# Optimization experiments

Hardware: AMD Instinct MI355X
Metric: run time of the kernel (lower is better)

Reference implementation:

```python
import jax, jax.numpy as jnp
import numpy as np

B, L, N = 16, 512, 32          # batch, seq_length, feature_size
E = 128                        # embed_size == frequency_size (number_frequency=1)
EMB = 8                        # embedding_dim
FCH = 64                       # fc_hidden_dim
H = 256                        # hidden_size
PRE = 96                       # pre_length
LAMBDA = 0.01                  # sparsity_threshold
SCALE = 0.02                   # init_scale


def softshrink(v, lambd=LAMBDA):
    return jnp.where(v > lambd, v - lambd, jnp.where(v < -lambd, v + lambd, 0.0))


def setup_inputs() -> dict:
    key = jax.random.key(0)
    ks = jax.random.split(key, 16)
    f32 = jnp.float32
    return {
        "x": jax.random.normal(ks[0], (B, L, N), f32),
        "emb": jax.random.normal(ks[1], (1, E), f32),
        "w0": SCALE * jax.random.normal(ks[2], (2, E, E), f32),
        "b0": SCALE * jax.random.normal(ks[3], (2, E), f32),
        "w1": SCALE * jax.random.normal(ks[4], (2, E, E), f32),
        "b1": SCALE * jax.random.normal(ks[5], (2, E), f32),
        "w2": SCALE * jax.random.normal(ks[6], (2, E, E), f32),
        "b2": SCALE * jax.random.normal(ks[7], (2, E), f32),
        "emb10": jax.random.normal(ks[8], (L, EMB), f32),
        "fc1_w": jax.random.normal(ks[9], (FCH, E * EMB), f32) / np.sqrt(E * EMB),
        "fc1_b": jnp.zeros((FCH,), f32),
        "fc2_w": jax.random.normal(ks[10], (H, FCH), f32) / np.sqrt(FCH),
        "fc2_b": jnp.zeros((H,), f32),
        "fc3_w": jax.random.normal(ks[11], (PRE, H), f32) / np.sqrt(H),
        "fc3_b": jnp.zeros((PRE,), f32),
    }


def _diag(w):
    # einsum 'bli,ii->bli' multiplies by the DIAGONAL of w only
    return jnp.diagonal(w, axis1=-2, axis2=-1)


def reference(x, emb, w0, b0, w1, b1, w2, b2, emb10,
              fc1_w, fc1_b, fc2_w, fc2_b, fc3_w, fc3_b):
    Bb = x.shape[0]
    xt = jnp.transpose(x, (0, 2, 1)).reshape(Bb, -1)          # [B, N*L]
    tok = xt[:, :, None] * emb                                 # [B, N*L, E]
    xf = jnp.fft.rfft(tok, axis=1, norm="ortho")               # [B, N*L//2+1, E] complex
    bias = xf

    # --- fourierGC (faithful to the torch op ordering, incl. o_real reuse) ---
    relu = jax.nn.relu
    d00, d01 = _diag(w0[0]), _diag(w0[1])
    o_r = relu(xf.real * d00 - xf.imag * d01 + b0[0])
    o_i = relu(xf.imag * d00 + xf.real * d01 + b0[1])
    prev = softshrink(jnp.stack([o_r, o_i], axis=-1))

    # middle layer (num_layers=3 -> one): note o_i uses the UPDATED o_r, as in torch
    d10, d11 = _diag(w1[0]), _diag(w1[1])
    o_r_new = relu(o_r * d10 - o_i * d11 + b1[0])
    o_i = relu(o_i * d10 + o_r_new * d11 + b1[1])
    o_r = o_r_new
    prev = softshrink(jnp.stack([o_r, o_i], axis=-1)) + prev

    # last layer
    d20, d21 = _diag(w2[0]), _diag(w2[1])
    o_r_new = relu(o_r * d20 - o_i * d21 + b2[0])
    o_i = relu(o_i * d20 + o_r_new * d21 + b2[1])
    z = softshrink(jnp.stack([o_r_new, o_i], axis=-1)) + prev
    zc = jax.lax.complex(z[..., 0], z[..., 1])

    xf = zc + bias
    xt = jnp.fft.irfft(xf, n=N * L, axis=1, norm="ortho")      # [B, N*L, E]
    xt = xt.reshape(Bb, N, L, E)
    xt = jnp.transpose(xt, (0, 1, 3, 2))                        # [B, N, E, L]
    h = jnp.matmul(xt, emb10)                                   # [B, N, E, EMB]
    h = h.reshape(Bb, N, E * EMB)

    lrelu = lambda v: jax.nn.leaky_relu(v, 0.01)
    h = lrelu(h @ fc1_w.T + fc1_b)
    h = lrelu(h @ fc2_w.T + fc2_b)
    out = h @ fc3_w.T + fc3_b                                   # [B, N, PRE]
    return out[:, 0, :]                                         # target_idx = 0
```

## Files before the change

### kernel.cpp

```cpp
#include <hip/hip_runtime.h>
#include <math.h>

#define Bsz   16
#define Lseq  512
#define Nfeat 32
#define E     128
#define EMB   8
#define FCH   64
#define Hd    256
#define PRE   96
#define M     16384
#define MH    8193
#define LAMBDA 0.01f

#define OFF_CS  0
#define OFF_P   131088

#define REV_M   6.103515625e-5f
#define REV_128 7.8125e-3f

__device__ __forceinline__ float sin_rev(float r) { return __builtin_amdgcn_sinf(r); }
__device__ __forceinline__ float cos_rev(float r) { return __builtin_amdgcn_cosf(r); }

__global__ __launch_bounds__(256, 4)
void k_cs(const float* __restrict__ emb10, float* __restrict__ ws) {
  __shared__ float e10T[Lseq * EMB];
  int bid = blockIdx.x, tid = threadIdx.x;
  for (int j = tid; j < Lseq * EMB; j += 256) {
    int t = j >> 3, m = j & 7;
    e10T[m * 512 + t] = emb10[j];
  }
  __syncthreads();
  int floc = tid >> 5, tl = tid & 31;
  #pragma unroll
  for (int ff = 0; ff < 4; ++ff) {
    int f = bid * 32 + ff * 8 + floc;
    float ca[EMB], sa[EMB];
    #pragma unroll
    for (int m = 0; m < EMB; ++m) { ca[m] = 0.f; sa[m] = 0.f; }
    #pragma unroll 4
    for (int it = 0; it < 16; ++it) {
      int t = tl + 32 * it;
      int k = (f * t) & (M - 1);
      float rv = (float)k * REV_M;
      float cc = cos_rev(rv), ss = sin_rev(rv);
      #pragma unroll
      for (int m = 0; m < EMB; ++m) {
        float ev = e10T[m * 512 + t];
        ca[m] = fmaf(cc, ev, ca[m]);
        sa[m] = fmaf(ss, ev, sa[m]);
      }
    }
    #pragma unroll
    for (int off = 16; off >= 1; off >>= 1) {
      #pragma unroll
      for (int m = 0; m < EMB; ++m) {
        ca[m] += __shfl_xor(ca[m], off, 64);
        sa[m] += __shfl_xor(sa[m], off, 64);
      }
    }
    if (tl == 0) {
      float wf = (f == 0) ? (1.0f / 128.0f) : (2.0f / 128.0f);
      float* o = ws + OFF_CS + f * 16;
      #pragma unroll
      for (int m = 0; m < EMB; ++m) { o[m] = ca[m] * wf; o[8 + m] = sa[m] * wf; }
    }
  }
  if (bid == 0 && tid < 64) {
    int m = tid & 7, g = tid >> 3;
    float p = 0.f;
    #pragma unroll 8
    for (int j = 0; j < 64; ++j) p += e10T[m * 512 + g + 8 * j];
    p = (g & 1) ? -p : p;
    p += __shfl_xor(p, 8, 64);
    p += __shfl_xor(p, 16, 64);
    p += __shfl_xor(p, 32, 64);
    if (g == 0) {
      ws[OFF_CS + 8192 * 16 + m] = p * (1.0f / 128.0f);
      ws[OFF_CS + 8192 * 16 + 8 + m] = 0.f;
    }
  }
}

#define XPAD(t) ((t) + ((t) >> 9))
__global__ __launch_bounds__(1024, 8)
void k_gcf(const float* __restrict__ x, const float* __restrict__ emb,
           const float* __restrict__ w0, const float* __restrict__ b0,
           const float* __restrict__ w1, const float* __restrict__ b1,
           const float* __restrict__ w2, const float* __restrict__ b2,
           float* __restrict__ ws) {
  __shared__ __align__(16) float xf[16416];
  __shared__ __align__(16) float2 Gs[4 * 132];
  float2* Xs = (float2*)xf;
  float* red = xf + 1024;
  int f1g = blockIdx.x, b = blockIdx.y, tid = threadIdx.x;
  int f1base = f1g * 4;
  {
    const float* xb = x + b * (Lseq * Nfeat);
    #pragma unroll
    for (int i = tid; i < Lseq * Nfeat; i += 1024) {
      int l = i >> 5, n = i & 31;
      xf[n * 513 + l] = xb[i];
    }
  }
  __syncthreads();
  if (tid < 512) {
    int f1loc = tid >> 7, t1 = tid & 127;
    int f1 = f1base + f1loc;
    float s1 = sin_rev((float)f1 * REV_128), c1 = cos_rev((float)f1 * REV_128);
    float c2 = c1 * c1 - s1 * s1, s2 = 2.f * s1 * c1;
    float cA = 1.f, sA = 0.f, cB = c1, sB = s1;
    float grA = 0.f, giA = 0.f, grB = 0.f, giB = 0.f;
    #pragma unroll 8
    for (int t2 = 0; t2 < 128; t2 += 2) {
      int ta = t1 + 128 * t2;
      float x0 = xf[XPAD(ta)], x1 = xf[XPAD(ta + 128)];
      grA = fmaf(x0, cA, grA); giA = fmaf(x0, -sA, giA);
      grB = fmaf(x1, cB, grB); giB = fmaf(x1, -sB, giB);
      float cn = cA * c2 - sA * s2; sA = sA * c2 + cA * s2; cA = cn;
      cn = cB * c2 - sB * s2;       sB = sB * c2 + cB * s2; cB = cn;
    }
    float gr = grA + grB, gi = giA + giB;
    float rv = (float)(f1 * t1) * REV_M;
    float sb = sin_rev(rv), cb = cos_rev(rv);
    Gs[f1loc * 132 + (t1 >> 5) * 33 + (t1 & 31)] =
        make_float2(gr * cb + gi * sb, gi * cb - gr * sb);
  }
  __syncthreads();
  {
    int w = tid >> 6, lane = tid & 63;
    int f1loc = w >> 2;
    int q = lane >> 4, f2 = ((w & 3) << 4) + (lane & 15);
    int r = (f2 * q) & 3;
    float c = (r == 0) ? 1.f : (r == 2) ? -1.f : 0.f;
    float s = (r == 1) ? 1.f : (r == 3) ? -1.f : 0.f;
    float s1 = sin_rev((float)f2 * REV_128), c1 = cos_rev((float)f2 * REV_128);
    float xr = 0.f, xi = 0.f;
    const float2* g = Gs + f1loc * 132 + q * 33;
    #pragma unroll 8
    for (int k = 0; k < 32; ++k) {
      float2 gv = g[k];
      xr = fmaf(gv.x, c, xr); xr = fmaf(gv.y, s, xr);
      xi = fmaf(gv.y, c, xi); xi = fmaf(-gv.x, s, xi);
      float cn = c * c1 - s * s1; s = s * c1 + c * s1; c = cn;
    }
    xr += __shfl_xor(xr, 16, 64); xi += __shfl_xor(xi, 16, 64);
    xr += __shfl_xor(xr, 32, 64); xi += __shfl_xor(xi, 32, 64);
    if (lane < 16) Xs[f1loc * 64 + f2] = make_float2(xr, xi);
    if (f1base == 0 && tid < 64) {
      int t1v = tid * 2;
      const float2* g0p = Gs + (t1v >> 5) * 33;
      float2 g0 = g0p[t1v & 31], g1 = g0p[(t1v & 31) + 1];
      float er = g0.x - g1.x, ei = g0.y - g1.y;
      #pragma unroll
      for (int off = 1; off <= 32; off <<= 1) {
        er += __shfl_xor(er, off, 64);
        ei += __shfl_xor(ei, off, 64);
      }
      if (tid == 0) Xs[256] = make_float2(er, ei);
    }
  }
  __syncthreads();
  int e = tid & 127, fh = tid >> 7;
  int nf = (f1base == 0) ? 257 : 256;
  float se  = emb[e] * (1.0f / 128.0f);
  float d00 = w0[e * 129], d01 = w0[E * E + e * 129];
  float c00 = b0[e],       c01 = b0[E + e];
  float d10 = w1[e * 129], d11 = w1[E * E + e * 129];
  float c10 = b1[e],       c11 = b1[E + e];
  float d20 = w2[e * 129], d21 = w2[E * E + e * 129];
  float c20 = b2[e],       c21 = b2[E + e];
  float acc[EMB];
  #pragma unroll
  for (int m = 0; m < EMB; ++m) acc[m] = 0.f;

  for (int i = fh; i < nf; i += 8) {
    int iu = __builtin_amdgcn_readfirstlane(i);
    int f = (iu == 256) ? 8192 : (f1base + (iu >> 6) + ((iu & 63) << 7));
    const float* cs = ws + OFF_CS + f * 16;
    float2 X = Xs[iu];
    float xr = X.x * se, xi = X.y * se;
    float or0 = fmaxf(fmaf(xr, d00, fmaf(-xi, d01, c00)), 0.f);
    float oi0 = fmaxf(fmaf(xi, d00, fmaf(xr, d01, c01)), 0.f);
    float pr = fmaxf(or0 - LAMBDA, 0.f), pi = fmaxf(oi0 - LAMBDA, 0.f);
    float or1 = fmaxf(fmaf(or0, d10, fmaf(-oi0, d11, c10)), 0.f);
    float oi1 = fmaxf(fmaf(oi0, d10, fmaf(or1, d11, c11)), 0.f);
    pr += fmaxf(or1 - LAMBDA, 0.f); pi += fmaxf(oi1 - LAMBDA, 0.f);
    float u2r = fmaf(or1, d20, fmaf(-oi1, d21, c20));
    float or2 = fmaxf(u2r, 0.f);
    float u2i = fmaf(oi1, d20, fmaf(or2, d21, c21));
    float zr = fmaxf(u2r - LAMBDA, 0.f) + pr;
    float zi = fmaxf(u2i - LAMBDA, 0.f) + pi;
    #pragma unroll
    for (int m = 0; m < EMB; ++m)
      acc[m] = fmaf(zr, cs[m], fmaf(-zi, cs[8 + m], acc[m]));
  }
  __syncthreads();
  if (fh > 0) {
    #pragma unroll
    for (int m = 0; m < EMB; ++m) red[(fh - 1) * 1024 + e * EMB + m] = acc[m];
  }
  __syncthreads();
  if (fh == 0) {
    #pragma unroll
    for (int j = 0; j < 7; ++j)
      #pragma unroll
      for (int m = 0; m < EMB; ++m) acc[m] += red[j * 1024 + e * EMB + m];
    float* P = ws + OFF_P + (f1g * 16 + b) * (E * EMB) + e * EMB;
    #pragma unroll
    for (int m = 0; m < EMB; ++m) P[m] = acc[m];
  }
}

__global__ __launch_bounds__(1024)
void k_fc(const float* __restrict__ x, const float* __restrict__ emb,
          const float* __restrict__ emb10,
          const float* __restrict__ fc1w, const float* __restrict__ fc1b,
          const float* __restrict__ fc2w, const float* __restrict__ fc2b,
          const float* __restrict__ fc3w, const float* __restrict__ fc3b,
          const float* __restrict__ ws, float* __restrict__ out) {
  int b = blockIdx.x;
  __shared__ float h0s[E * EMB];
  __shared__ float h1s[FCH];
  __shared__ float h2s[Hd];
  __shared__ float hxs[EMB];
  __shared__ float scratch[1024];
  int tid = threadIdx.x;
  int lane = tid & 63, w = tid >> 6;
  {
    int m = tid & 7, g = tid >> 3;
    float p = 0.f;
    #pragma unroll
    for (int l = g; l < Lseq; l += 128)
      p = fmaf(x[b * (Lseq * Nfeat) + l * Nfeat], emb10[l * EMB + m], p);
    scratch[tid] = p;
  }
  const float* P = ws + OFF_P + b * (E * EMB) + tid;
  float a = 0.f;
  #pragma unroll
  for (int c = 0; c < 32; ++c) a += P[c * (Bsz * E * EMB)];
  __syncthreads();
  if (tid < 8) {
    float s = 0.f;
    #pragma unroll 16
    for (int g = 0; g < 128; ++g) s += scratch[g * 8 + tid];
    hxs[tid] = s;
  }
  __syncthreads();
  h0s[tid] = a + emb[tid >> 3] * hxs[tid & 7];
  __syncthreads();
  #pragma unroll
  for (int oo = 0; oo < 4; ++oo) {
    int o = oo * 16 + w;
    const float* wr = fc1w + o * (E * EMB);
    float acc = 0.f;
    #pragma unroll
    for (int j = 0; j < 16; ++j) acc = fmaf(h0s[lane + 64 * j], wr[lane + 64 * j], acc);
    #pragma unroll
    for (int off = 32; off >= 1; off >>= 1) acc += __shfl_xor(acc, off, 64);
    if (lane == 0) { float v = acc + fc1b[o]; h1s[o] = v > 0.f ? v : 0.01f * v; }
  }
  __syncthreads();
  #pragma unroll
  for (int oo = 0; oo < 16; ++oo) {
    int o = oo * 16 + w;
    float acc = h1s[lane] * fc2w[o * FCH + lane];
    #pragma unroll
    for (int off = 32; off >= 1; off >>= 1) acc += __shfl_xor(acc, off, 64);
    if (lane == 0) { float v = acc + fc2b[o]; h2s[o] = v > 0.f ? v : 0.01f * v; }
  }
  __syncthreads();
  #pragma unroll
  for (int oo = 0; oo < 6; ++oo) {
    int o = oo * 16 + w;
    const float* wr = fc3w + o * Hd;
    float acc = 0.f;
    #pragma unroll
    for (int j = 0; j < 4; ++j) acc = fmaf(h2s[lane + 64 * j], wr[lane + 64 * j], acc);
    #pragma unroll
    for (int off = 32; off >= 1; off >>= 1) acc += __shfl_xor(acc, off, 64);
    if (lane == 0) out[b * PRE + o] = acc + fc3b[o];
  }
}

extern "C" void kernel_launch(void* const* d_in, const int* in_sizes, int n_in,
                              void* d_out, int out_size, void* d_ws, size_t ws_size,
                              hipStream_t stream) {
  const float* x     = (const float*)d_in[0];
  const float* emb   = (const float*)d_in[1];
  const float* w0    = (const float*)d_in[2];
  const float* b0    = (const float*)d_in[3];
  const float* w1    = (const float*)d_in[4];
  const float* b1    = (const float*)d_in[5];
  const float* w2    = (const float*)d_in[6];
  const float* b2    = (const float*)d_in[7];
  const float* emb10 = (const float*)d_in[8];
  const float* fc1w  = (const float*)d_in[9];
  const float* fc1b  = (const float*)d_in[10];
  const float* fc2w  = (const float*)d_in[11];
  const float* fc2b  = (const float*)d_in[12];
  const float* fc3w  = (const float*)d_in[13];
  const float* fc3b  = (const float*)d_in[14];
  float* ws  = (float*)d_ws;
  float* out = (float*)d_out;

  k_cs<<<dim3(256), 256, 0, stream>>>(emb10, ws);
  k_gcf<<<dim3(32, Bsz), 1024, 0, stream>>>(x, emb, w0, b0, w1, b1, w2, b2, ws);
  k_fc<<<dim3(Bsz), 1024, 0, stream>>>(x, emb, emb10, fc1w, fc1b, fc2w, fc2b,
                                       fc3w, fc3b, ws, out);
}
```

Baseline: 151.3 us.

## Split first DFT stage across all threads and unroll gc loop statically

The first-stage twiddle DFT is split across both halves of the 1024-thread block, each half covering 64 of the 128 t2 steps. Partial sums are combined through shared memory, with a sign fix for the odd-half phase offset. The per-frequency graph-conv loop is fully unrolled with compile-time indexing and wave-uniform addressing. The reduction scratch is padded to stride 9 to reduce LDS bank conflicts. This keeps all threads busy in the DFT phase at the cost of an extra shared-memory round trip and two more barriers.

```diff
diff --git a/kernel.cpp b/kernel.cpp
--- a/kernel.cpp
+++ b/kernel.cpp
@@ -91,6 +91,7 @@
            float* __restrict__ ws) {
   __shared__ __align__(16) float xf[16416];
   __shared__ __align__(16) float2 Gs[4 * 132];
+  float2* part = (float2*)xf;
   float2* Xs = (float2*)xf;
   float* red = xf + 1024;
   int f1g = blockIdx.x, b = blockIdx.y, tid = threadIdx.x;
@@ -104,23 +105,36 @@
     }
   }
   __syncthreads();
-  if (tid < 512) {
-    int f1loc = tid >> 7, t1 = tid & 127;
-    int f1 = f1base + f1loc;
+  float pgr, pgi;
+  int h = tid >> 9, f1loc4 = (tid >> 7) & 3, t1f = tid & 127;
+  {
+    int f1 = f1base + f1loc4;
     float s1 = sin_rev((float)f1 * REV_128), c1 = cos_rev((float)f1 * REV_128);
     float c2 = c1 * c1 - s1 * s1, s2 = 2.f * s1 * c1;
     float cA = 1.f, sA = 0.f, cB = c1, sB = s1;
     float grA = 0.f, giA = 0.f, grB = 0.f, giB = 0.f;
+    int t2base = h << 6;
     #pragma unroll 8
-    for (int t2 = 0; t2 < 128; t2 += 2) {
-      int ta = t1 + 128 * t2;
+    for (int j = 0; j < 64; j += 2) {
+      int ta = t1f + 128 * (t2base + j);
       float x0 = xf[XPAD(ta)], x1 = xf[XPAD(ta + 128)];
       grA = fmaf(x0, cA, grA); giA = fmaf(x0, -sA, giA);
       grB = fmaf(x1, cB, grB); giB = fmaf(x1, -sB, giB);
       float cn = cA * c2 - sA * s2; sA = sA * c2 + cA * s2; cA = cn;
       cn = cB * c2 - sB * s2;       sB = sB * c2 + cB * s2; cB = cn;
     }
-    float gr = grA + grB, gi = giA + giB;
+    float sign = ((f1 & h) & 1) ? -1.f : 1.f;
+    pgr = (grA + grB) * sign;
+    pgi = (giA + giB) * sign;
+  }
+  __syncthreads();
+  part[h * 512 + f1loc4 * 128 + t1f] = make_float2(pgr, pgi);
+  __syncthreads();
+  if (tid < 512) {
+    int f1loc = tid >> 7, t1 = tid & 127;
+    int f1 = f1base + f1loc;
+    float2 A = part[f1loc * 128 + t1], B = part[512 + f1loc * 128 + t1];
+    float gr = A.x + B.x, gi = A.y + B.y;
     float rv = (float)(f1 * t1) * REV_M;
     float sb = sin_rev(rv), cb = cos_rev(rv);
     Gs[f1loc * 132 + (t1 >> 5) * 33 + (t1 & 31)] =
@@ -161,8 +175,8 @@
     }
   }
   __syncthreads();
-  int e = tid & 127, fh = tid >> 7;
-  int nf = (f1base == 0) ? 257 : 256;
+  int e = tid & 127;
+  int fhu = __builtin_amdgcn_readfirstlane(tid >> 7);
   float se  = emb[e] * (1.0f / 128.0f);
   float d00 = w0[e * 129], d01 = w0[E * E + e * 129];
   float c00 = b0[e],       c01 = b0[E + e];
@@ -174,11 +188,7 @@
   #pragma unroll
   for (int m = 0; m < EMB; ++m) acc[m] = 0.f;
 
-  for (int i = fh; i < nf; i += 8) {
-    int iu = __builtin_amdgcn_readfirstlane(i);
-    int f = (iu == 256) ? 8192 : (f1base + (iu >> 6) + ((iu & 63) << 7));
-    const float* cs = ws + OFF_CS + f * 16;
-    float2 X = Xs[iu];
+  auto gc_point = [&](float2 X, const float* cs) {
     float xr = X.x * se, xi = X.y * se;
     float or0 = fmaxf(fmaf(xr, d00, fmaf(-xi, d01, c00)), 0.f);
     float oi0 = fmaxf(fmaf(xi, d00, fmaf(xr, d01, c01)), 0.f);
@@ -194,18 +204,32 @@
     #pragma unroll
     for (int m = 0; m < EMB; ++m)
       acc[m] = fmaf(zr, cs[m], fmaf(-zi, cs[8 + m], acc[m]));
-  }
-  __syncthreads();
-  if (fh > 0) {
-    #pragma unroll
-    for (int m = 0; m < EMB; ++m) red[(fh - 1) * 1024 + e * EMB + m] = acc[m];
-  }
-  __syncthreads();
-  if (fh == 0) {
+  };
+
+  {
+    const float* csb = ws + OFF_CS + ((f1base + 128 * fhu) << 4);
+    #pragma unroll
+    for (int f1loc = 0; f1loc < 4; ++f1loc) {
+      #pragma unroll
+      for (int j = 0; j < 8; ++j) {
+        gc_point(Xs[f1loc * 64 + fhu + 8 * j],
+                 csb + (f1loc << 4) + (j << 14));
+      }
+    }
+    if (f1base == 0 && fhu == 0)
+      gc_point(Xs[256], ws + OFF_CS + 8192 * 16);
+  }
+  __syncthreads();
+  if (fhu > 0) {
+    #pragma unroll
+    for (int m = 0; m < EMB; ++m) red[(fhu - 1) * 1152 + e * 9 + m] = acc[m];
+  }
+  __syncthreads();
+  if (fhu == 0) {
     #pragma unroll
     for (int j = 0; j < 7; ++j)
       #pragma unroll
-      for (int m = 0; m < EMB; ++m) acc[m] += red[j * 1024 + e * EMB + m];
+      for (int m = 0; m < EMB; ++m) acc[m] += red[j * 1152 + e * 9 + m];
     float* P = ws + OFF_P + (f1g * 16 + b) * (E * EMB) + e * EMB;
     #pragma unroll
     for (int m = 0; m < EMB; ++m) P[m] = acc[m];
```

New measurement: 151.5 us. Within noise of the previous version (+0.1%).
